# Kernel optimization log

Measured on AMD Instinct MI355X. Metric: run time of the kernel, lower is better.

The kernel has to match this reference:

```python
import jax, jax.numpy as jnp
import numpy as np

N, IN_DIM, HID, OUT = 8192, 512, 256, 64
NEG_INF = -9e15


def setup_inputs() -> dict:
    key = jax.random.key(0)
    ks = jax.random.split(key, 7)
    X = jax.random.normal(ks[0], (N, IN_DIM), dtype=jnp.float32)
    A = jax.random.randint(ks[1], (N, N), 0, 2, dtype=jnp.int32)
    # fc1 (Linear): kaiming-uniform-ish init, exact dist irrelevant for correctness
    W1 = jax.random.normal(ks[2], (IN_DIM, HID), dtype=jnp.float32) / np.sqrt(IN_DIM)
    b1 = jnp.zeros((HID,), dtype=jnp.float32)
    # attention vector a: xavier_uniform(gain=1.414) on shape (2*HID, 1)
    lim = 1.414 * np.sqrt(6.0 / (2 * HID + 1))
    a = jax.random.uniform(ks[3], (2 * HID, 1), minval=-lim, maxval=lim, dtype=jnp.float32)
    Omega = jax.random.normal(ks[4], (HID, OUT), dtype=jnp.float32) * np.sqrt(2.0 / (HID + OUT))
    beta = jnp.zeros((OUT,), dtype=jnp.float32)
    return {"X": X, "A": A, "W1": W1, "b1": b1, "a": a, "Omega": Omega, "beta": beta}


def reference(X, A, W1, b1, a, Omega, beta):
    H1 = X @ W1 + b1                      # [N, HID]
    # score(i,j) = leakyrelu(a[:HID].H1_i + a[HID:].H1_j) -- computed via broadcast,
    # avoiding the O(N^2 * 2*HID) concat the torch code materializes.
    a1 = a[:HID, 0]                       # [HID]
    a2 = a[HID:, 0]                       # [HID]
    e = jax.nn.leaky_relu((H1 @ a1)[:, None] + (H1 @ a2)[None, :], negative_slope=0.2)  # [N, N]
    e = jnp.where(A > 0, e, NEG_INF)
    attention = jax.nn.softmax(e, axis=1)  # dropout_rate=0.0 -> identity
    H2 = attention @ H1                    # [N, HID]
    return jax.nn.sigmoid(H2 @ Omega + beta)  # [N, OUT]
```

## Files before the change

### kernel.cpp

```cpp
#include <hip/hip_runtime.h>
#include <hip/hip_bf16.h>


typedef float f32x4 __attribute__((ext_vector_type(4)));
typedef short s16x8 __attribute__((ext_vector_type(8)));

#define NN 8192
#define INDIM 512
#define HIDD 256
#define OUTD 64

static __device__ __forceinline__ short f2bf(float x) {
    __hip_bfloat16 h = __float2bfloat16(x);
    return __builtin_bit_cast(short, h);
}

static __device__ __forceinline__ unsigned pk2bf(float a, float b) {
    unsigned ha = (unsigned)(unsigned short)f2bf(a);
    unsigned hb = (unsigned)(unsigned short)f2bf(b);
    return ha | (hb << 16);
}

static __device__ __forceinline__ void split_bf(float x, short& hi, short& lo) {
    short h = f2bf(x);
    unsigned int hb = ((unsigned int)(unsigned short)h) << 16;
    float hf = __builtin_bit_cast(float, hb);
    hi = h;
    lo = f2bf(x - hf);
}

__global__ void k_prepX(const float* __restrict__ X, short* __restrict__ XBhi) {
    int t = blockIdx.x * 256 + threadIdx.x;
    int r = t >> 9, k = t & 511;
    XBhi[(r >> 4) * 8192 + (k >> 3) * 128 + (r & 15) * 8 + (k & 7)] = f2bf(X[t]);
}

__global__ void k_prepW(const float* __restrict__ W1,
                        short* __restrict__ WBhi, short* __restrict__ WBlo) {
    int t = blockIdx.x * 256 + threadIdx.x;
    int k = t >> 8, n = t & 255;
    short h, l; split_bf(W1[t], h, l);
    int idx = (n >> 4) * 8192 + (k >> 3) * 128 + (n & 15) * 8 + (k & 7);
    WBhi[idx] = h;
    WBlo[idx] = l;
}

__global__ void __launch_bounds__(256) k_packA(const int* __restrict__ A,
                                               unsigned long long* __restrict__ Apk64) {
    const int tid = threadIdx.x;
    int f = blockIdx.x * 256 + tid;
#pragma unroll 4
    for (int it = 0; it < 128; ++it) {
        int a = A[(size_t)f];
        unsigned long long m = __ballot(a > 0);
        if ((tid & 63) == 0) Apk64[f >> 6] = m;
        f += 524288;
    }
}

__global__ void __launch_bounds__(256, 2)
k_h1(const short* __restrict__ XBhi, const short* __restrict__ WBhi,
     const short* __restrict__ WBlo, const float* __restrict__ b1,
     const float* __restrict__ avec, unsigned short* __restrict__ H1TB,
     float* __restrict__ alw, float* __restrict__ bew, float* __restrict__ uvw) {
    __shared__ float s1p[4][16];
    __shared__ float s2p[4][16];
    const int tid = threadIdx.x;
    const int wn = tid >> 6, lane = tid & 63;
    const int q = lane >> 4, m16 = lane & 15;
    const int blk = blockIdx.x;

    f32x4 zero4 = {0.f, 0.f, 0.f, 0.f};
    f32x4 acc[4];
#pragma unroll
    for (int nt = 0; nt < 4; ++nt) acc[nt] = zero4;

    const short* xh = XBhi + blk * 8192 + q * 128 + m16 * 8;
    const short* wh = WBhi + wn * 4 * 8192 + q * 128 + m16 * 8;
    const short* wl = WBlo + wn * 4 * 8192 + q * 128 + m16 * 8;

    for (int c = 0; c < 16; ++c) {
        s16x8 ahi = *(const s16x8*)(xh + c * 512);
#pragma unroll
        for (int nt = 0; nt < 4; ++nt) {
            s16x8 bhi = *(const s16x8*)(wh + nt * 8192 + c * 512);
            s16x8 blo = *(const s16x8*)(wl + nt * 8192 + c * 512);
            acc[nt] = __builtin_amdgcn_mfma_f32_16x16x32_bf16(ahi, bhi, acc[nt], 0, 0, 0);
            acc[nt] = __builtin_amdgcn_mfma_f32_16x16x32_bf16(ahi, blo, acc[nt], 0, 0, 0);
        }
    }

    float p1[4] = {0.f, 0.f, 0.f, 0.f};
    float p2[4] = {0.f, 0.f, 0.f, 0.f};
#pragma unroll
    for (int nt = 0; nt < 4; ++nt) {
        const int col = wn * 64 + nt * 16 + m16;
        const float b1v = b1[col];
        const float a1v = avec[col];
        const float a2v = avec[HIDD + col];
        float v0 = acc[nt][0] + b1v;
        float v1 = acc[nt][1] + b1v;
        float v2 = acc[nt][2] + b1v;
        float v3 = acc[nt][3] + b1v;
        ushort4 us;
        us.x = (unsigned short)f2bf(v0);
        us.y = (unsigned short)f2bf(v1);
        us.z = (unsigned short)f2bf(v2);
        us.w = (unsigned short)f2bf(v3);
        const int idx = ((wn * 4 + nt) * 1024 + blk * 2 + (q >> 1)) * 128
                        + m16 * 8 + (q & 1) * 4;
        *(ushort4*)(H1TB + idx) = us;
        p1[0] += v0 * a1v; p1[1] += v1 * a1v; p1[2] += v2 * a1v; p1[3] += v3 * a1v;
        p2[0] += v0 * a2v; p2[1] += v1 * a2v; p2[2] += v2 * a2v; p2[3] += v3 * a2v;
    }
#pragma unroll
    for (int off = 1; off < 16; off <<= 1) {
#pragma unroll
        for (int r = 0; r < 4; ++r) {
            p1[r] += __shfl_xor(p1[r], off);
            p2[r] += __shfl_xor(p2[r], off);
        }
    }
    if (m16 == 0) {
#pragma unroll
        for (int r = 0; r < 4; ++r) {
            s1p[wn][q * 4 + r] = p1[r];
            s2p[wn][q * 4 + r] = p2[r];
        }
    }
    __syncthreads();
    if (tid < 16) {
        const int i = blk * 16 + tid;
        float s1 = s1p[0][tid] + s1p[1][tid] + s1p[2][tid] + s1p[3][tid];
        float s2 = s2p[0][tid] + s2p[1][tid] + s2p[2][tid] + s2p[3][tid];
        alw[i] = expf(s1);
        bew[i] = expf(0.2f * s1);
        uvw[2 * i]     = expf(s2);
        uvw[2 * i + 1] = expf(0.2f * s2);
    }
}

__global__ void __launch_bounds__(256, 3)
k_attn_ns(const unsigned int* __restrict__ Apk, const unsigned short* __restrict__ H1TB,
          const float* __restrict__ alw, const float* __restrict__ bew,
          const float* __restrict__ uvw,
          float* __restrict__ H2p, float* __restrict__ Zp, int kslog) {
    const int tid = threadIdx.x;
    const int wn = tid >> 6, lane = tid & 63;
    const int q = lane >> 4, m16 = lane & 15;
    const int ksn = 1 << kslog;
    const int ks = blockIdx.x & (ksn - 1);
    const int mb = blockIdx.x >> kslog;
    const int row0 = mb * 32 + m16, row1 = row0 + 16;
    const float al0 = alw[row0], be0 = bew[row0];
    const float al1 = alw[row1], be1 = bew[row1];
    const int jbase = ks << (13 - kslog);
    const int chunks = 64 >> kslog;

    const unsigned int* Ap0 = Apk + row0 * 256 + (jbase >> 5);
    const unsigned int* Ap1 = Apk + row1 * 256 + (jbase >> 5);
    const float* uvp = uvw + 2 * (jbase + q * 8);
    const unsigned short* Hp = H1TB
        + ((size_t)(wn * 4) * 1024 + (jbase >> 3) + q) * 128 + m16 * 8;

    f32x4 zero4 = {0.f, 0.f, 0.f, 0.f};
    f32x4 acc[4][2];
#pragma unroll
    for (int nt = 0; nt < 4; ++nt) { acc[nt][0] = zero4; acc[nt][1] = zero4; }
    float z0 = 0.f, z1 = 0.f;

    uint4 aw0 = *(const uint4*)(Ap0);
    uint4 aw1 = *(const uint4*)(Ap1);

    for (int c = 0; c < chunks; ++c) {
        uint4 nx0, nx1;
        if (c + 1 < chunks) {
            nx0 = *(const uint4*)(Ap0 + 4);
            nx1 = *(const uint4*)(Ap1 + 4);
        }
        unsigned wda0[4] = {aw0.x, aw0.y, aw0.z, aw0.w};
        unsigned wda1[4] = {aw1.x, aw1.y, aw1.z, aw1.w};
#pragma unroll
        for (int u = 0; u < 4; ++u) {
            const int t = c * 4 + u;
            const unsigned b0 = (wda0[u] >> (q * 8)) & 0xFFu;
            const unsigned b1 = (wda1[u] >> (q * 8)) & 0xFFu;
            float4 uv0 = *(const float4*)(uvp + t * 64);
            float4 uv1 = *(const float4*)(uvp + t * 64 + 4);
            float4 uv2 = *(const float4*)(uvp + t * 64 + 8);
            float4 uv3 = *(const float4*)(uvp + t * 64 + 12);
            float w0[8], w1[8];
            w0[0] = (b0 & 1u)   ? fmaxf(al0 * uv0.x, be0 * uv0.y) : 0.f;
            w0[1] = (b0 & 2u)   ? fmaxf(al0 * uv0.z, be0 * uv0.w) : 0.f;
            w0[2] = (b0 & 4u)   ? fmaxf(al0 * uv1.x, be0 * uv1.y) : 0.f;
            w0[3] = (b0 & 8u)   ? fmaxf(al0 * uv1.z, be0 * uv1.w) : 0.f;
            w0[4] = (b0 & 16u)  ? fmaxf(al0 * uv2.x, be0 * uv2.y) : 0.f;
            w0[5] = (b0 & 32u)  ? fmaxf(al0 * uv2.z, be0 * uv2.w) : 0.f;
            w0[6] = (b0 & 64u)  ? fmaxf(al0 * uv3.x, be0 * uv3.y) : 0.f;
            w0[7] = (b0 & 128u) ? fmaxf(al0 * uv3.z, be0 * uv3.w) : 0.f;
            w1[0] = (b1 & 1u)   ? fmaxf(al1 * uv0.x, be1 * uv0.y) : 0.f;
            w1[1] = (b1 & 2u)   ? fmaxf(al1 * uv0.z, be1 * uv0.w) : 0.f;
            w1[2] = (b1 & 4u)   ? fmaxf(al1 * uv1.x, be1 * uv1.y) : 0.f;
            w1[3] = (b1 & 8u)   ? fmaxf(al1 * uv1.z, be1 * uv1.w) : 0.f;
            w1[4] = (b1 & 16u)  ? fmaxf(al1 * uv2.x, be1 * uv2.y) : 0.f;
            w1[5] = (b1 & 32u)  ? fmaxf(al1 * uv2.z, be1 * uv2.w) : 0.f;
            w1[6] = (b1 & 64u)  ? fmaxf(al1 * uv3.x, be1 * uv3.y) : 0.f;
            w1[7] = (b1 & 128u) ? fmaxf(al1 * uv3.z, be1 * uv3.w) : 0.f;
            z0 += (w0[0] + w0[1] + w0[2] + w0[3]) + (w0[4] + w0[5] + w0[6] + w0[7]);
            z1 += (w1[0] + w1[1] + w1[2] + w1[3]) + (w1[4] + w1[5] + w1[6] + w1[7]);

            int4 ai0 = {(int)pk2bf(w0[0], w0[1]), (int)pk2bf(w0[2], w0[3]),
                        (int)pk2bf(w0[4], w0[5]), (int)pk2bf(w0[6], w0[7])};
            int4 ai1 = {(int)pk2bf(w1[0], w1[1]), (int)pk2bf(w1[2], w1[3]),
                        (int)pk2bf(w1[4], w1[5]), (int)pk2bf(w1[6], w1[7])};
            s16x8 af0 = __builtin_bit_cast(s16x8, ai0);
            s16x8 af1 = __builtin_bit_cast(s16x8, ai1);
#pragma unroll
            for (int nt = 0; nt < 4; ++nt) {
                s16x8 bf = *(const s16x8*)(Hp + (size_t)nt * 131072 + t * 512);
                acc[nt][0] = __builtin_amdgcn_mfma_f32_16x16x32_bf16(af0, bf, acc[nt][0], 0, 0, 0);
                acc[nt][1] = __builtin_amdgcn_mfma_f32_16x16x32_bf16(af1, bf, acc[nt][1], 0, 0, 0);
            }
        }
        aw0 = nx0; aw1 = nx1;
        Ap0 += 4; Ap1 += 4;
    }

    z0 += __shfl_xor(z0, 16); z0 += __shfl_xor(z0, 32);
    z1 += __shfl_xor(z1, 16); z1 += __shfl_xor(z1, 32);
    if (wn == 0 && q == 0) {
        Zp[ks * NN + row0] = z0;
        Zp[ks * NN + row1] = z1;
    }

    float* H2s = H2p + (size_t)ks * (NN * HIDD / 1) / (1)
                 ;
    H2s = H2p + (size_t)ks * 2097152;
#pragma unroll
    for (int nt = 0; nt < 4; ++nt) {
        const int col = wn * 64 + nt * 16 + m16;
#pragma unroll
        for (int rg = 0; rg < 2; ++rg) {
            const int rowb = mb * 32 + rg * 16 + q * 4;
#pragma unroll
            for (int r = 0; r < 4; ++r)
                H2s[(size_t)(rowb + r) * HIDD + col] = acc[nt][rg][r];
        }
    }
}

__global__ void __launch_bounds__(256)
k_out(const float* __restrict__ H2p, const float* __restrict__ Zp,
      const float* __restrict__ Omega, const float* __restrict__ beta,
      float* __restrict__ out, int ksn) {
    __shared__ float om[HIDD * OUTD];
    const int tid = threadIdx.x;
    for (int idx = tid; idx < HIDD * OUTD; idx += 256) om[idx] = Omega[idx];
    __syncthreads();
    const int wave = tid >> 6, o = tid & 63;
    const int i0 = blockIdx.x * 32 + wave * 8;
    float accv[8] = {0.f, 0.f, 0.f, 0.f, 0.f, 0.f, 0.f, 0.f};
    for (int s = 0; s < ksn; ++s) {
        const float* Hs = H2p + (size_t)s * 2097152;
        for (int c = 0; c < HIDD; c += 4) {
            const float o0 = om[(c + 0) * OUTD + o];
            const float o1 = om[(c + 1) * OUTD + o];
            const float o2 = om[(c + 2) * OUTD + o];
            const float o3 = om[(c + 3) * OUTD + o];
#pragma unroll
            for (int r = 0; r < 8; ++r) {
                float4 h = *(const float4*)(Hs + (size_t)(i0 + r) * HIDD + c);
                accv[r] = fmaf(h.x, o0, fmaf(h.y, o1, fmaf(h.z, o2, fmaf(h.w, o3, accv[r]))));
            }
        }
    }
    const float bv = beta[o];
#pragma unroll
    for (int r = 0; r < 8; ++r) {
        float z = 0.f;
        for (int s = 0; s < ksn; ++s) z += Zp[s * NN + i0 + r];
        const float logit = accv[r] / z + bv;
        out[(size_t)(i0 + r) * OUTD + o] = 1.0f / (1.0f + expf(-logit));
    }
}

extern "C" void kernel_launch(void* const* d_in, const int* in_sizes, int n_in,
                              void* d_out, int out_size, void* d_ws, size_t ws_size,
                              hipStream_t stream) {
    const float* X     = (const float*)d_in[0];
    const int*   A     = (const int*)d_in[1];
    const float* W1    = (const float*)d_in[2];
    const float* b1    = (const float*)d_in[3];
    const float* avec  = (const float*)d_in[4];
    const float* Omega = (const float*)d_in[5];
    const float* beta  = (const float*)d_in[6];
    float* out = (float*)d_out;
    char* ws = (char*)d_ws;

    int kslog = (ws_size >= 46923776ull) ? 2 : (ws_size >= 30081024ull) ? 1 : 0;
    const int ksn = 1 << kslog;

    size_t off = 0;
    unsigned short* H1TB = (unsigned short*)(ws + off); off += 4194304;
    unsigned int*   Apk  = (unsigned int*)(ws + off);   off += 8388608;
    float* H2p = (float*)(ws + off);
    short* XBhi = (short*)(ws + off);
    off += (size_t)ksn * 8388608;
    float* Zp  = (float*)(ws + off); off += (size_t)ksn * 32768;
    short* WBhi = (short*)(ws + off); off += 262144;
    short* WBlo = (short*)(ws + off); off += 262144;
    float* alw = (float*)(ws + off); off += 32768;
    float* bew = (float*)(ws + off); off += 32768;
    float* uvw = (float*)(ws + off); off += 65536;

    k_prepX<<<16384, 256, 0, stream>>>(X, XBhi);
    k_prepW<<<512, 256, 0, stream>>>(W1, WBhi, WBlo);
    k_h1<<<512, 256, 0, stream>>>(XBhi, WBhi, WBlo, b1, avec, H1TB, alw, bew, uvw);
    k_packA<<<2048, 256, 0, stream>>>(A, (unsigned long long*)Apk);
    k_attn_ns<<<256 * ksn, 256, 0, stream>>>(Apk, H1TB, alw, bew, uvw, H2p, Zp, kslog);
    k_out<<<256, 256, 0, stream>>>(H2p, Zp, Omega, beta, out, ksn);
}
```

Before: 590.5 us.

## Restructure attention kernel so each wave covers all hidden columns for its rows

The attention kernel now gives each wave its own 32 rows and all 256 hidden columns (16 column tiles), instead of splitting columns across four waves that share rows. This removes the fourfold recomputation of mask decoding, softmax weights and bf16 packing per row, but raises accumulator register pressure (128 floats per lane) and lowers occupancy. The X to bf16 conversion is folded into the H1 GEMM, removing the separate prep kernel and its workspace traffic. The workspace threshold logic also allows an 8-way K split when enough memory is available.

Measured after the change: 813.5 us. 37.8% more time.

```diff
diff --git a/kernel.cpp b/kernel.cpp
--- a/kernel.cpp
+++ b/kernel.cpp
@@ -27,12 +27,6 @@
     float hf = __builtin_bit_cast(float, hb);
     hi = h;
     lo = f2bf(x - hf);
-}
-
-__global__ void k_prepX(const float* __restrict__ X, short* __restrict__ XBhi) {
-    int t = blockIdx.x * 256 + threadIdx.x;
-    int r = t >> 9, k = t & 511;
-    XBhi[(r >> 4) * 8192 + (k >> 3) * 128 + (r & 15) * 8 + (k & 7)] = f2bf(X[t]);
 }
 
 __global__ void k_prepW(const float* __restrict__ W1,
@@ -59,7 +53,7 @@
 }
 
 __global__ void __launch_bounds__(256, 2)
-k_h1(const short* __restrict__ XBhi, const short* __restrict__ WBhi,
+k_h1(const float* __restrict__ X, const short* __restrict__ WBhi,
      const short* __restrict__ WBlo, const float* __restrict__ b1,
      const float* __restrict__ avec, unsigned short* __restrict__ H1TB,
      float* __restrict__ alw, float* __restrict__ bew, float* __restrict__ uvw) {
@@ -75,12 +69,17 @@
 #pragma unroll
     for (int nt = 0; nt < 4; ++nt) acc[nt] = zero4;
 
-    const short* xh = XBhi + blk * 8192 + q * 128 + m16 * 8;
+    const float* Xrow = X + (size_t)(blk * 16 + m16) * INDIM + q * 8;
     const short* wh = WBhi + wn * 4 * 8192 + q * 128 + m16 * 8;
     const short* wl = WBlo + wn * 4 * 8192 + q * 128 + m16 * 8;
 
     for (int c = 0; c < 16; ++c) {
-        s16x8 ahi = *(const s16x8*)(xh + c * 512);
+        float4 xa = *(const float4*)(Xrow + c * 32);
+        float4 xb = *(const float4*)(Xrow + c * 32 + 4);
+        float xs[8] = {xa.x, xa.y, xa.z, xa.w, xb.x, xb.y, xb.z, xb.w};
+        s16x8 ahi;
+#pragma unroll
+        for (int j = 0; j < 8; ++j) ahi[j] = f2bf(xs[j]);
 #pragma unroll
         for (int nt = 0; nt < 4; ++nt) {
             s16x8 bhi = *(const s16x8*)(wh + nt * 8192 + c * 512);
@@ -140,18 +139,18 @@
     }
 }
 
-__global__ void __launch_bounds__(256, 3)
-k_attn_ns(const unsigned int* __restrict__ Apk, const unsigned short* __restrict__ H1TB,
+__global__ void __launch_bounds__(256, 2)
+k_attn_rs(const unsigned int* __restrict__ Apk, const unsigned short* __restrict__ H1TB,
           const float* __restrict__ alw, const float* __restrict__ bew,
           const float* __restrict__ uvw,
           float* __restrict__ H2p, float* __restrict__ Zp, int kslog) {
     const int tid = threadIdx.x;
-    const int wn = tid >> 6, lane = tid & 63;
+    const int wave = tid >> 6, lane = tid & 63;
     const int q = lane >> 4, m16 = lane & 15;
     const int ksn = 1 << kslog;
     const int ks = blockIdx.x & (ksn - 1);
     const int mb = blockIdx.x >> kslog;
-    const int row0 = mb * 32 + m16, row1 = row0 + 16;
+    const int row0 = mb * 128 + wave * 32 + m16, row1 = row0 + 16;
     const float al0 = alw[row0], be0 = bew[row0];
     const float al1 = alw[row1], be1 = bew[row1];
     const int jbase = ks << (13 - kslog);
@@ -160,13 +159,12 @@
     const unsigned int* Ap0 = Apk + row0 * 256 + (jbase >> 5);
     const unsigned int* Ap1 = Apk + row1 * 256 + (jbase >> 5);
     const float* uvp = uvw + 2 * (jbase + q * 8);
-    const unsigned short* Hp = H1TB
-        + ((size_t)(wn * 4) * 1024 + (jbase >> 3) + q) * 128 + m16 * 8;
+    const unsigned short* Hp = H1TB + ((size_t)(jbase >> 3) + q) * 128 + m16 * 8;
 
     f32x4 zero4 = {0.f, 0.f, 0.f, 0.f};
-    f32x4 acc[4][2];
-#pragma unroll
-    for (int nt = 0; nt < 4; ++nt) { acc[nt][0] = zero4; acc[nt][1] = zero4; }
+    f32x4 acc[16][2];
+#pragma unroll
+    for (int nt = 0; nt < 16; ++nt) { acc[nt][0] = zero4; acc[nt][1] = zero4; }
     float z0 = 0.f, z1 = 0.f;
 
     uint4 aw0 = *(const uint4*)(Ap0);
@@ -174,7 +172,8 @@
 
     for (int c = 0; c < chunks; ++c) {
         uint4 nx0, nx1;
-        if (c + 1 < chunks) {
+        const bool pf = (c + 1 < chunks);
+        if (pf) {
             nx0 = *(const uint4*)(Ap0 + 4);
             nx1 = *(const uint4*)(Ap1 + 4);
         }
@@ -216,32 +215,30 @@
             s16x8 af0 = __builtin_bit_cast(s16x8, ai0);
             s16x8 af1 = __builtin_bit_cast(s16x8, ai1);
 #pragma unroll
-            for (int nt = 0; nt < 4; ++nt) {
+            for (int nt = 0; nt < 16; ++nt) {
                 s16x8 bf = *(const s16x8*)(Hp + (size_t)nt * 131072 + t * 512);
                 acc[nt][0] = __builtin_amdgcn_mfma_f32_16x16x32_bf16(af0, bf, acc[nt][0], 0, 0, 0);
                 acc[nt][1] = __builtin_amdgcn_mfma_f32_16x16x32_bf16(af1, bf, acc[nt][1], 0, 0, 0);
             }
         }
-        aw0 = nx0; aw1 = nx1;
+        if (pf) { aw0 = nx0; aw1 = nx1; }
         Ap0 += 4; Ap1 += 4;
     }
 
     z0 += __shfl_xor(z0, 16); z0 += __shfl_xor(z0, 32);
     z1 += __shfl_xor(z1, 16); z1 += __shfl_xor(z1, 32);
-    if (wn == 0 && q == 0) {
+    if (q == 0) {
         Zp[ks * NN + row0] = z0;
         Zp[ks * NN + row1] = z1;
     }
 
-    float* H2s = H2p + (size_t)ks * (NN * HIDD / 1) / (1)
-                 ;
-    H2s = H2p + (size_t)ks * 2097152;
-#pragma unroll
-    for (int nt = 0; nt < 4; ++nt) {
-        const int col = wn * 64 + nt * 16 + m16;
+    float* H2s = H2p + (size_t)ks * 2097152;
+#pragma unroll
+    for (int nt = 0; nt < 16; ++nt) {
+        const int col = nt * 16 + m16;
 #pragma unroll
         for (int rg = 0; rg < 2; ++rg) {
-            const int rowb = mb * 32 + rg * 16 + q * 4;
+            const int rowb = mb * 128 + wave * 32 + rg * 16 + q * 4;
 #pragma unroll
             for (int r = 0; r < 4; ++r)
                 H2s[(size_t)(rowb + r) * HIDD + col] = acc[nt][rg][r];
@@ -297,15 +294,15 @@
     float* out = (float*)d_out;
     char* ws = (char*)d_ws;
 
-    int kslog = (ws_size >= 46923776ull) ? 2 : (ws_size >= 30081024ull) ? 1 : 0;
+    int kslog = (ws_size >= 81000000ull) ? 3
+              : (ws_size >= 47000000ull) ? 2
+              : (ws_size >= 30200000ull) ? 1 : 0;
     const int ksn = 1 << kslog;
 
     size_t off = 0;
     unsigned short* H1TB = (unsigned short*)(ws + off); off += 4194304;
     unsigned int*   Apk  = (unsigned int*)(ws + off);   off += 8388608;
-    float* H2p = (float*)(ws + off);
-    short* XBhi = (short*)(ws + off);
-    off += (size_t)ksn * 8388608;
+    float* H2p = (float*)(ws + off); off += (size_t)ksn * 8388608;
     float* Zp  = (float*)(ws + off); off += (size_t)ksn * 32768;
     short* WBhi = (short*)(ws + off); off += 262144;
     short* WBlo = (short*)(ws + off); off += 262144;
@@ -313,10 +310,9 @@
     float* bew = (float*)(ws + off); off += 32768;
     float* uvw = (float*)(ws + off); off += 65536;
 
-    k_prepX<<<16384, 256, 0, stream>>>(X, XBhi);
     k_prepW<<<512, 256, 0, stream>>>(W1, WBhi, WBlo);
-    k_h1<<<512, 256, 0, stream>>>(XBhi, WBhi, WBlo, b1, avec, H1TB, alw, bew, uvw);
+    k_h1<<<512, 256, 0, stream>>>(X, WBhi, WBlo, b1, avec, H1TB, alw, bew, uvw);
     k_packA<<<2048, 256, 0, stream>>>(A, (unsigned long long*)Apk);
-    k_attn_ns<<<256 * ksn, 256, 0, stream>>>(Apk, H1TB, alw, bew, uvw, H2p, Zp, kslog);
+    k_attn_rs<<<64 << kslog, 256, 0, stream>>>(Apk, H1TB, alw, bew, uvw, H2p, Zp, kslog);
     k_out<<<256, 256, 0, stream>>>(H2p, Zp, Omega, beta, out, ksn);
 }
```
